# Kernel optimization log

Measured on AMD Instinct MI355X. Metric: run time of the kernel, lower is better.

The kernel has to match this reference:

```python
import jax, jax.numpy as jnp
import numpy as np

N = 4096
F = 1024
UNITS = 128
HEADS = 8
MASK_VAL = -10000000000.0  # -1e10, matches the source
LEAKY_ALPHA = 0.2


def setup_inputs() -> dict:
    key = jax.random.key(0)
    ks = jax.random.split(key, 6)
    X = jax.random.normal(ks[0], (1, N, F), dtype=jnp.float32)
    # Binary adjacency with self-loops (the layer expects self-loops preprocessed in).
    u = jax.random.uniform(ks[1], (N, N), dtype=jnp.float32)
    A = ((u < 0.01).astype(jnp.float32) + jnp.eye(N, dtype=jnp.float32))
    A = jnp.minimum(A, 1.0)[None]  # [1, N, N]
    W = jax.random.normal(ks[2], (HEADS, F, UNITS), dtype=jnp.float32) * (1.0 / np.sqrt(F))
    a_self = jax.random.normal(ks[3], (HEADS, UNITS), dtype=jnp.float32) * 0.1
    a_neigh = jax.random.normal(ks[4], (HEADS, UNITS), dtype=jnp.float32) * 0.1
    b = jnp.zeros((HEADS, UNITS), dtype=jnp.float32)
    return {"X": X, "A": A, "W": W, "a_self": a_self, "a_neigh": a_neigh, "b": b}


def reference(X, A, W, a_self, a_neigh, b):
    x = X[0]   # [N, F]
    adj = A[0]  # [N, N]
    # Per-head feature projection: [H, N, U]
    feat = jnp.einsum("nf,hfu->hnu", x, W)
    # Additive attention logits: e_ij = leaky_relu(a_s . h_i + a_n . h_j)
    s = jnp.einsum("hnu,hu->hn", feat, a_self)    # [H, N]
    t = jnp.einsum("hnu,hu->hn", feat, a_neigh)   # [H, N]
    dense = s[:, :, None] + t[:, None, :]          # [H, N, N]
    dense = jax.nn.leaky_relu(dense, negative_slope=LEAKY_ALPHA)
    # Mask non-edges with -1e10 (dense += -1e10 * (1 - A))
    dense = dense + MASK_VAL * (1.0 - adj)[None]
    attn = jax.nn.softmax(dense, axis=-1)          # [H, N, N]
    # Weighted aggregation + bias: [H, N, U]
    h = jnp.einsum("hnm,hmu->hnu", attn, feat) + b[:, None, :]
    # Concat heads: [N, H*U]
    out = jnp.transpose(h, (1, 0, 2)).reshape(N, HEADS * UNITS)
    out = jax.nn.relu(out)
    return out[None]  # [1, N, H*U]
```

## Files before the change

kernel.cpp:

```cpp
#include <hip/hip_runtime.h>


constexpr int NN = 4096;
constexpr int FF = 1024;
constexpr int HH = 8;
constexpr int UU = 128;
constexpr int CC = HH * UU;
constexpr int MAXDEG = 128;
constexpr float ALPHA = 0.2f;

typedef __attribute__((ext_vector_type(8))) short short8;
typedef __attribute__((ext_vector_type(4))) float f32x4;

__device__ inline unsigned short f2bf(float x) {
  unsigned u = __float_as_uint(x);
  return (unsigned short)((u + 0x7fffu + ((u >> 16) & 1u)) >> 16);
}
__device__ inline float bf2f(unsigned short h) { return __uint_as_float(((unsigned)h) << 16); }

__global__ __launch_bounds__(256) void convert_X(const float* __restrict__ X,
                                                 unsigned short* __restrict__ Xhi,
                                                 unsigned short* __restrict__ Xlo) {
  size_t base = ((size_t)blockIdx.x * 256 + threadIdx.x) * 8;
  float4 v0 = *(const float4*)(X + base);
  float4 v1 = *(const float4*)(X + base + 4);
  float xs[8] = {v0.x, v0.y, v0.z, v0.w, v1.x, v1.y, v1.z, v1.w};
  short8 vh, vl;
#pragma unroll
  for (int e = 0; e < 8; ++e) {
    unsigned short hb = f2bf(xs[e]);
    vh[e] = (short)hb;
    vl[e] = (short)f2bf(xs[e] - bf2f(hb));
  }
  *(short8*)(Xhi + base) = vh;
  *(short8*)(Xlo + base) = vl;
}

__global__ __launch_bounds__(256) void transposeW(const float* __restrict__ W,
                                                  unsigned short* __restrict__ WT) {
  const int h = blockIdx.x >> 3, ft = blockIdx.x & 7;
  const int f0 = ft * 128;
  __shared__ unsigned short hiT[128][136];
  __shared__ unsigned short loT[128][136];
  const int tid = threadIdx.x;
#pragma unroll
  for (int it = 0; it < 16; ++it) {
    int idx = it * 256 + tid;
    int r = idx >> 5;
    int u4 = idx & 31;
    float4 v = *(const float4*)(W + (size_t)h * FF * UU + (size_t)(f0 + r) * UU + u4 * 4);
    float xs[4] = {v.x, v.y, v.z, v.w};
#pragma unroll
    for (int e = 0; e < 4; ++e) {
      unsigned short hb = f2bf(xs[e]);
      hiT[u4 * 4 + e][r] = hb;
      loT[u4 * 4 + e][r] = f2bf(xs[e] - bf2f(hb));
    }
  }
  __syncthreads();
#pragma unroll
  for (int it = 0; it < 8; ++it) {
    int idx = it * 256 + tid;
    int u = idx >> 4, f8 = idx & 15;
    short8 vh = *(const short8*)&hiT[u][f8 * 8];
    short8 vl = *(const short8*)&loT[u][f8 * 8];
    size_t o = (size_t)h * UU * FF + (size_t)u * FF + f0 + f8 * 8;
    *(short8*)(WT + o) = vh;
    *(short8*)(WT + (size_t)HH * UU * FF + o) = vl;
  }
}

__global__ __launch_bounds__(256) void build_csr(const float* __restrict__ A,
                                                 int* __restrict__ deg,
                                                 int* __restrict__ idx) {
  const int i = blockIdx.x;
  const int tid = threadIdx.x;
  const int lane = tid & 63;
  __shared__ int cnt;
  if (tid == 0) cnt = 0;
  __syncthreads();
  const float4* row = reinterpret_cast<const float4*>(A + (size_t)i * NN);
  for (int c = tid; c < NN / 4; c += 256) {
    float4 v = row[c];
    unsigned long long m0 = __ballot(v.x > 0.5f);
    unsigned long long m1 = __ballot(v.y > 0.5f);
    unsigned long long m2 = __ballot(v.z > 0.5f);
    unsigned long long m3 = __ballot(v.w > 0.5f);
    int wtot = __popcll(m0) + __popcll(m1) + __popcll(m2) + __popcll(m3);
    if (wtot) {
      int base = 0;
      if (lane == 0) base = atomicAdd(&cnt, wtot);
      base = __shfl(base, 0);
      unsigned long long lt = (1ull << lane) - 1;
      int c0 = __popcll(m0), c1 = __popcll(m1), c2 = __popcll(m2);
      int o;
      o = base + __popcll(m0 & lt);
      if (v.x > 0.5f && o < MAXDEG) idx[i * MAXDEG + o] = c * 4 + 0;
      o = base + c0 + __popcll(m1 & lt);
      if (v.y > 0.5f && o < MAXDEG) idx[i * MAXDEG + o] = c * 4 + 1;
      o = base + c0 + c1 + __popcll(m2 & lt);
      if (v.z > 0.5f && o < MAXDEG) idx[i * MAXDEG + o] = c * 4 + 2;
      o = base + c0 + c1 + c2 + __popcll(m3 & lt);
      if (v.w > 0.5f && o < MAXDEG) idx[i * MAXDEG + o] = c * 4 + 3;
    }
  }
  __syncthreads();
  if (tid == 0) deg[i] = cnt > MAXDEG ? MAXDEG : cnt;
}

constexpr int NTILE = 48;

__global__ __launch_bounds__(512) void gemm_mfma(const unsigned short* __restrict__ Xhi,
                                                 const unsigned short* __restrict__ Xlo,
                                                 const unsigned short* __restrict__ WT,
                                                 float* __restrict__ feat) {
  __shared__ char lds[2][32768];
  const int tid = threadIdx.x;
  const int w = tid >> 6, l = tid & 63;
  const int h = blockIdx.x & 7;
  const int row0 = (blockIdx.x >> 3) * 128;
  const int wr = w >> 2, wc = w & 3;

  const int lr = l >> 3;
  const int sk = ((l & 7) ^ lr) * 8;
  const unsigned short* WTh = WT + (size_t)h * UU * FF;

  f32x4 acc[4][2] = {};

  auto stage = [&](int t, int buf) {
    int s = t >> 4, kt = t & 15;
    const unsigned short* As = ((s == 1) ? Xlo : Xhi) +
        (size_t)(row0 + w * 16 + lr) * FF + kt * 64 + sk;
    const unsigned short* Bs = WTh + ((s == 2) ? (size_t)HH * UU * FF : (size_t)0) +
        (size_t)(w * 16 + lr) * FF + kt * 64 + sk;
    char* la = &lds[buf][w * 2048];
    char* lb = &lds[buf][16384 + w * 2048];
#pragma unroll
    for (int dr = 0; dr < 2; ++dr) {
      __builtin_amdgcn_global_load_lds(
          (const __attribute__((address_space(1))) unsigned int*)(As + (size_t)dr * 8 * FF),
          (__attribute__((address_space(3))) unsigned int*)(la + dr * 1024), 16, 0, 0);
      __builtin_amdgcn_global_load_lds(
          (const __attribute__((address_space(1))) unsigned int*)(Bs + (size_t)dr * 8 * FF),
          (__attribute__((address_space(3))) unsigned int*)(lb + dr * 1024), 16, 0, 0);
    }
  };

  const int arow = wr * 64 + (l & 15);
  const int bcol = wc * 32 + (l & 15);
  const int kswz = (l & 7) << 4;
  const int kb = (l >> 4) * 16;

  auto compute = [&](int buf) {
#pragma unroll
    for (int ks = 0; ks < 2; ++ks) {
      const int ko = ks * 64 + kb;
      short8 a[4], b[2];
#pragma unroll
      for (int mi = 0; mi < 4; ++mi)
        a[mi] = *(const short8*)(&lds[buf][(arow + mi * 16) * 128 + (ko ^ kswz)]);
#pragma unroll
      for (int ni = 0; ni < 2; ++ni)
        b[ni] = *(const short8*)(&lds[buf][16384 + (bcol + ni * 16) * 128 + (ko ^ kswz)]);
#pragma unroll
      for (int mi = 0; mi < 4; ++mi)
#pragma unroll
        for (int ni = 0; ni < 2; ++ni)
          acc[mi][ni] = __builtin_amdgcn_mfma_f32_16x16x32_bf16(a[mi], b[ni],
                                                                acc[mi][ni], 0, 0, 0);
    }
  };

  stage(0, 0);
  __syncthreads();
  for (int tt = 0; tt < NTILE; ++tt) {
    if (tt + 1 < NTILE) stage(tt + 1, (tt + 1) & 1);
    compute(tt & 1);
    __syncthreads();
  }

  const int ccol = h * 128 + wc * 32 + (l & 15);
  const int crow0 = row0 + wr * 64 + (l >> 4) * 4;
#pragma unroll
  for (int mi = 0; mi < 4; ++mi)
#pragma unroll
    for (int ni = 0; ni < 2; ++ni)
#pragma unroll
      for (int r = 0; r < 4; ++r)
        feat[(size_t)(crow0 + mi * 16 + r) * CC + ccol + ni * 16] = acc[mi][ni][r];
}

__global__ __launch_bounds__(256) void st_kernel(const float* __restrict__ feat,
                                                 const float* __restrict__ a_self,
                                                 const float* __restrict__ a_neigh,
                                                 float* __restrict__ s_arr,
                                                 float* __restrict__ t_arr) {
  const int n = blockIdx.x;
  const int tid = threadIdx.x;
  const int wave = tid >> 6, lane = tid & 63;
  const float* frow = feat + (size_t)n * CC;
#pragma unroll
  for (int hh = 0; hh < 2; ++hh) {
    int h = wave * 2 + hh;
    int c0 = h * UU + lane;
    float f0 = frow[c0], f1 = frow[c0 + 64];
    float vs = f0 * a_self[c0] + f1 * a_self[c0 + 64];
    float vt = f0 * a_neigh[c0] + f1 * a_neigh[c0 + 64];
#pragma unroll
    for (int o = 32; o > 0; o >>= 1) {
      vs += __shfl_xor(vs, o);
      vt += __shfl_xor(vt, o);
    }
    if (lane == 0) {
      s_arr[h * NN + n] = vs;
      t_arr[h * NN + n] = vt;
    }
  }
}

__global__ __launch_bounds__(128) void aggregate(const float* __restrict__ feat,
                                                 const float* __restrict__ s_arr,
                                                 const float* __restrict__ t_arr,
                                                 const int* __restrict__ deg_arr,
                                                 const int* __restrict__ idx_arr,
                                                 const float* __restrict__ bias,
                                                 float* __restrict__ out) {
  const int b = blockIdx.x;
  const int h = b >> 12;
  const int i = b & (NN - 1);
  const int tid = threadIdx.x;
  __shared__ float p[MAXDEG];
  __shared__ int jj[MAXDEG];
  __shared__ float wred[2][2];

  const int deg = deg_arr[i];
  const float si = s_arr[h * NN + i];
  float e = -1e30f;
  if (tid < deg) {
    int j = idx_arr[i * MAXDEG + tid];
    jj[tid] = j;
    float x = si + t_arr[h * NN + j];
    e = x > 0.0f ? x : ALPHA * x;
  }
  float m = e;
#pragma unroll
  for (int o = 32; o > 0; o >>= 1) m = fmaxf(m, __shfl_xor(m, o));
  if ((tid & 63) == 0) wred[0][tid >> 6] = m;
  __syncthreads();
  m = fmaxf(wred[0][0], wred[0][1]);

  float pe = (tid < deg) ? expf(e - m) : 0.0f;
  p[tid] = pe;
  float ssum = pe;
#pragma unroll
  for (int o = 32; o > 0; o >>= 1) ssum += __shfl_xor(ssum, o);
  if ((tid & 63) == 0) wred[1][tid >> 6] = ssum;
  __syncthreads();
  const float inv = 1.0f / (wred[1][0] + wred[1][1]);

  const float* fh = feat + h * UU + tid;
  float acc = 0.0f;
  int k = 0;
  for (; k + 3 < deg; k += 4) {
    float p0 = p[k], p1 = p[k + 1], p2 = p[k + 2], p3 = p[k + 3];
    int j0 = jj[k], j1 = jj[k + 1], j2 = jj[k + 2], j3 = jj[k + 3];
    acc += p0 * fh[(size_t)j0 * CC] + p1 * fh[(size_t)j1 * CC] +
           p2 * fh[(size_t)j2 * CC] + p3 * fh[(size_t)j3 * CC];
  }
  for (; k < deg; ++k) acc += p[k] * fh[(size_t)jj[k] * CC];

  float o = acc * inv + bias[h * UU + tid];
  out[(size_t)i * CC + h * UU + tid] = fmaxf(o, 0.0f);
}

extern "C" void kernel_launch(void* const* d_in, const int* in_sizes, int n_in,
                              void* d_out, int out_size, void* d_ws, size_t ws_size,
                              hipStream_t stream) {
  const float* X       = (const float*)d_in[0];
  const float* A       = (const float*)d_in[1];
  const float* W       = (const float*)d_in[2];
  const float* a_self  = (const float*)d_in[3];
  const float* a_neigh = (const float*)d_in[4];
  const float* bias    = (const float*)d_in[5];
  float* out = (float*)d_out;

  float* feat = (float*)d_ws;
  unsigned short* Xhi = (unsigned short*)(feat + (size_t)NN * CC);
  unsigned short* Xlo = Xhi + (size_t)NN * FF;
  unsigned short* WT  = Xlo + (size_t)NN * FF;
  float* s_arr = (float*)(WT + (size_t)2 * HH * UU * FF);
  float* t_arr = s_arr + HH * NN;
  int* deg = (int*)(t_arr + HH * NN);
  int* idx = deg + NN;

  hipLaunchKernelGGL(convert_X, dim3(NN * FF / (256 * 8)), dim3(256), 0, stream, X, Xhi, Xlo);
  hipLaunchKernelGGL(transposeW, dim3(64), dim3(256), 0, stream, W, WT);
  hipLaunchKernelGGL(build_csr, dim3(NN), dim3(256), 0, stream, A, deg, idx);
  hipLaunchKernelGGL(gemm_mfma, dim3(256), dim3(512), 0, stream, Xhi, Xlo, WT, feat);
  hipLaunchKernelGGL(st_kernel, dim3(NN), dim3(256), 0, stream, feat, a_self, a_neigh, s_arr, t_arr);
  hipLaunchKernelGGL(aggregate, dim3(HH * NN), dim3(128), 0, stream,
                     feat, s_arr, t_arr, deg, idx, bias, out);
}
```

Baseline: 223.8 us.

## Fuse attention score dots into GEMM epilogue and aggregate all heads per node

Result: slower. 254.0 us (+13.5%).

```diff
diff --git a/kernel.cpp b/kernel.cpp
--- a/kernel.cpp
+++ b/kernel.cpp
@@ -113,7 +113,11 @@
 __global__ __launch_bounds__(512) void gemm_mfma(const unsigned short* __restrict__ Xhi,
                                                  const unsigned short* __restrict__ Xlo,
                                                  const unsigned short* __restrict__ WT,
-                                                 float* __restrict__ feat) {
+                                                 const float* __restrict__ a_self,
+                                                 const float* __restrict__ a_neigh,
+                                                 float* __restrict__ feat,
+                                                 float* __restrict__ s_arr,
+                                                 float* __restrict__ t_arr) {
   __shared__ char lds[2][32768];
   const int tid = threadIdx.x;
   const int w = tid >> 6, l = tid & 63;
@@ -188,89 +192,122 @@
 #pragma unroll
       for (int r = 0; r < 4; ++r)
         feat[(size_t)(crow0 + mi * 16 + r) * CC + ccol + ni * 16] = acc[mi][ni][r];
-}
-
-__global__ __launch_bounds__(256) void st_kernel(const float* __restrict__ feat,
-                                                 const float* __restrict__ a_self,
-                                                 const float* __restrict__ a_neigh,
-                                                 float* __restrict__ s_arr,
-                                                 float* __restrict__ t_arr) {
-  const int n = blockIdx.x;
-  const int tid = threadIdx.x;
-  const int wave = tid >> 6, lane = tid & 63;
-  const float* frow = feat + (size_t)n * CC;
-#pragma unroll
-  for (int hh = 0; hh < 2; ++hh) {
-    int h = wave * 2 + hh;
-    int c0 = h * UU + lane;
-    float f0 = frow[c0], f1 = frow[c0 + 64];
-    float vs = f0 * a_self[c0] + f1 * a_self[c0 + 64];
-    float vt = f0 * a_neigh[c0] + f1 * a_neigh[c0 + 64];
-#pragma unroll
-    for (int o = 32; o > 0; o >>= 1) {
-      vs += __shfl_xor(vs, o);
-      vt += __shfl_xor(vt, o);
-    }
-    if (lane == 0) {
-      s_arr[h * NN + n] = vs;
-      t_arr[h * NN + n] = vt;
-    }
-  }
-}
-
-__global__ __launch_bounds__(128) void aggregate(const float* __restrict__ feat,
+
+  const int u0 = wc * 32 + (l & 15);
+  const float as0 = a_self[h * UU + u0], as1 = a_self[h * UU + u0 + 16];
+  const float an0 = a_neigh[h * UU + u0], an1 = a_neigh[h * UU + u0 + 16];
+  float ps[16], pt[16];
+#pragma unroll
+  for (int mi = 0; mi < 4; ++mi)
+#pragma unroll
+    for (int r = 0; r < 4; ++r) {
+      ps[mi * 4 + r] = acc[mi][0][r] * as0 + acc[mi][1][r] * as1;
+      pt[mi * 4 + r] = acc[mi][0][r] * an0 + acc[mi][1][r] * an1;
+    }
+#pragma unroll
+  for (int mask = 1; mask <= 8; mask <<= 1)
+#pragma unroll
+    for (int q = 0; q < 16; ++q) {
+      ps[q] += __shfl_xor(ps[q], mask);
+      pt[q] += __shfl_xor(pt[q], mask);
+    }
+  float(*sred)[4] = (float(*)[4]) & lds[0][0];
+  float(*tred)[4] = (float(*)[4]) & lds[0][2048];
+  if ((l & 15) == 0) {
+#pragma unroll
+    for (int mi = 0; mi < 4; ++mi)
+#pragma unroll
+      for (int r = 0; r < 4; ++r) {
+        int rl = wr * 64 + mi * 16 + (l >> 4) * 4 + r;
+        sred[rl][wc] = ps[mi * 4 + r];
+        tred[rl][wc] = pt[mi * 4 + r];
+      }
+  }
+  __syncthreads();
+  if (tid < 128) {
+    float sv = sred[tid][0] + sred[tid][1] + sred[tid][2] + sred[tid][3];
+    float tv = tred[tid][0] + tred[tid][1] + tred[tid][2] + tred[tid][3];
+    s_arr[h * NN + row0 + tid] = sv;
+    t_arr[h * NN + row0 + tid] = tv;
+  }
+}
+
+__global__ __launch_bounds__(256) void aggregate(const float* __restrict__ feat,
                                                  const float* __restrict__ s_arr,
                                                  const float* __restrict__ t_arr,
                                                  const int* __restrict__ deg_arr,
                                                  const int* __restrict__ idx_arr,
                                                  const float* __restrict__ bias,
                                                  float* __restrict__ out) {
-  const int b = blockIdx.x;
-  const int h = b >> 12;
-  const int i = b & (NN - 1);
+  const int i = blockIdx.x;
   const int tid = threadIdx.x;
-  __shared__ float p[MAXDEG];
+  const int g = tid >> 5;
+  const int l32 = tid & 31;
   __shared__ int jj[MAXDEG];
-  __shared__ float wred[2][2];
+  __shared__ float p_lds[HH][MAXDEG];
+  __shared__ float inv_lds[HH];
 
   const int deg = deg_arr[i];
-  const float si = s_arr[h * NN + i];
-  float e = -1e30f;
-  if (tid < deg) {
-    int j = idx_arr[i * MAXDEG + tid];
-    jj[tid] = j;
-    float x = si + t_arr[h * NN + j];
-    e = x > 0.0f ? x : ALPHA * x;
-  }
-  float m = e;
-#pragma unroll
-  for (int o = 32; o > 0; o >>= 1) m = fmaxf(m, __shfl_xor(m, o));
-  if ((tid & 63) == 0) wred[0][tid >> 6] = m;
-  __syncthreads();
-  m = fmaxf(wred[0][0], wred[0][1]);
-
-  float pe = (tid < deg) ? expf(e - m) : 0.0f;
-  p[tid] = pe;
-  float ssum = pe;
-#pragma unroll
-  for (int o = 32; o > 0; o >>= 1) ssum += __shfl_xor(ssum, o);
-  if ((tid & 63) == 0) wred[1][tid >> 6] = ssum;
-  __syncthreads();
-  const float inv = 1.0f / (wred[1][0] + wred[1][1]);
-
-  const float* fh = feat + h * UU + tid;
-  float acc = 0.0f;
+  if (tid < MAXDEG && tid < deg) jj[tid] = idx_arr[i * MAXDEG + tid];
+  __syncthreads();
+
+  const float si = s_arr[g * NN + i];
+  float e[4];
+#pragma unroll
+  for (int c = 0; c < 4; ++c) {
+    int k = l32 + c * 32;
+    if (k < deg) {
+      float x = si + t_arr[g * NN + jj[k]];
+      e[c] = x > 0.0f ? x : ALPHA * x;
+    } else {
+      e[c] = -3e38f;
+    }
+  }
+  float m = fmaxf(fmaxf(e[0], e[1]), fmaxf(e[2], e[3]));
+#pragma unroll
+  for (int mask = 1; mask <= 16; mask <<= 1) m = fmaxf(m, __shfl_xor(m, mask));
+  float pv[4], sum = 0.0f;
+#pragma unroll
+  for (int c = 0; c < 4; ++c) {
+    pv[c] = __expf(e[c] - m);
+    sum += pv[c];
+  }
+#pragma unroll
+  for (int mask = 1; mask <= 16; mask <<= 1) sum += __shfl_xor(sum, mask);
+#pragma unroll
+  for (int c = 0; c < 4; ++c) p_lds[g][l32 + c * 32] = pv[c];
+  if (l32 == 0) inv_lds[g] = 1.0f / sum;
+  __syncthreads();
+
+  const float* fbase = feat + tid * 4;
+  float ax = 0.0f, ay = 0.0f, az = 0.0f, aw = 0.0f;
   int k = 0;
   for (; k + 3 < deg; k += 4) {
-    float p0 = p[k], p1 = p[k + 1], p2 = p[k + 2], p3 = p[k + 3];
     int j0 = jj[k], j1 = jj[k + 1], j2 = jj[k + 2], j3 = jj[k + 3];
-    acc += p0 * fh[(size_t)j0 * CC] + p1 * fh[(size_t)j1 * CC] +
-           p2 * fh[(size_t)j2 * CC] + p3 * fh[(size_t)j3 * CC];
-  }
-  for (; k < deg; ++k) acc += p[k] * fh[(size_t)jj[k] * CC];
-
-  float o = acc * inv + bias[h * UU + tid];
-  out[(size_t)i * CC + h * UU + tid] = fmaxf(o, 0.0f);
+    float p0 = p_lds[g][k], p1 = p_lds[g][k + 1];
+    float p2 = p_lds[g][k + 2], p3 = p_lds[g][k + 3];
+    float4 v0 = *(const float4*)(fbase + (size_t)j0 * CC);
+    float4 v1 = *(const float4*)(fbase + (size_t)j1 * CC);
+    float4 v2 = *(const float4*)(fbase + (size_t)j2 * CC);
+    float4 v3 = *(const float4*)(fbase + (size_t)j3 * CC);
+    ax += p0 * v0.x + p1 * v1.x + p2 * v2.x + p3 * v3.x;
+    ay += p0 * v0.y + p1 * v1.y + p2 * v2.y + p3 * v3.y;
+    az += p0 * v0.z + p1 * v1.z + p2 * v2.z + p3 * v3.z;
+    aw += p0 * v0.w + p1 * v1.w + p2 * v2.w + p3 * v3.w;
+  }
+  for (; k < deg; ++k) {
+    float pk = p_lds[g][k];
+    float4 v = *(const float4*)(fbase + (size_t)jj[k] * CC);
+    ax += pk * v.x; ay += pk * v.y; az += pk * v.z; aw += pk * v.w;
+  }
+  const float inv = inv_lds[g];
+  const float4 b4 = *(const float4*)(bias + tid * 4);
+  float4 o;
+  o.x = fmaxf(ax * inv + b4.x, 0.0f);
+  o.y = fmaxf(ay * inv + b4.y, 0.0f);
+  o.z = fmaxf(az * inv + b4.z, 0.0f);
+  o.w = fmaxf(aw * inv + b4.w, 0.0f);
+  *(float4*)(out + (size_t)i * CC + tid * 4) = o;
 }
 
 extern "C" void kernel_launch(void* const* d_in, const int* in_sizes, int n_in,
@@ -296,8 +333,8 @@
   hipLaunchKernelGGL(convert_X, dim3(NN * FF / (256 * 8)), dim3(256), 0, stream, X, Xhi, Xlo);
   hipLaunchKernelGGL(transposeW, dim3(64), dim3(256), 0, stream, W, WT);
   hipLaunchKernelGGL(build_csr, dim3(NN), dim3(256), 0, stream, A, deg, idx);
-  hipLaunchKernelGGL(gemm_mfma, dim3(256), dim3(512), 0, stream, Xhi, Xlo, WT, feat);
-  hipLaunchKernelGGL(st_kernel, dim3(NN), dim3(256), 0, stream, feat, a_self, a_neigh, s_arr, t_arr);
-  hipLaunchKernelGGL(aggregate, dim3(HH * NN), dim3(128), 0, stream,
+  hipLaunchKernelGGL(gemm_mfma, dim3(256), dim3(512), 0, stream,
+                     Xhi, Xlo, WT, a_self, a_neigh, feat, s_arr, t_arr);
+  hipLaunchKernelGGL(aggregate, dim3(NN), dim3(256), 0, stream,
                      feat, s_arr, t_arr, deg, idx, bias, out);
 }
```
